# Kernel optimization log

Hardware: AMD Instinct MI355X
Metric: run time of the kernel (lower is better)

Reference implementation:

```python
import jax, jax.numpy as jnp
import numpy as np
import math

B, C, H, W = 16, 128, 64, 64

def _conv3(x, w, b):
    # 3x3 conv, padding=1 (SAME), NCHW / OIHW
    y = jax.lax.conv_general_dilated(x, w, window_strides=(1, 1), padding='SAME',
                                     dimension_numbers=('NCHW', 'OIHW', 'NCHW'))
    return y + b[None, :, None, None]

def setup_inputs() -> dict:
    key = jax.random.key(0)
    ks = jax.random.split(key, 12)
    s = 0.02
    inp = {
        'F_in': jax.random.normal(ks[0], (B, C, H, W), dtype=jnp.float32),
        'Pspe': jax.random.normal(ks[1], (B, C, C), dtype=jnp.float32),
        'q_w': jax.random.normal(ks[2], (C, C, 3, 3), dtype=jnp.float32) * s,
        'q_b': jnp.zeros((C,), dtype=jnp.float32),
        'k_w': jax.random.normal(ks[3], (C, C, 3, 3), dtype=jnp.float32) * s,
        'k_b': jnp.zeros((C,), dtype=jnp.float32),
        'v_w': jax.random.normal(ks[4], (C, C, 3, 3), dtype=jnp.float32) * s,
        'v_b': jnp.zeros((C,), dtype=jnp.float32),
        'f1_w': jax.random.normal(ks[5], (C, C, 3, 3), dtype=jnp.float32) * s,
        'f1_b': jnp.zeros((C,), dtype=jnp.float32),
        'f2_w': jax.random.normal(ks[6], (C, C, 3, 3), dtype=jnp.float32) * s,
        'f2_b': jnp.zeros((C,), dtype=jnp.float32),
    }
    return inp

def reference(F_in, Pspe, q_w, q_b, k_w, k_b, v_w, v_b, f1_w, f1_b, f2_w, f2_b):
    b, c, h, w = F_in.shape
    hw = h * w
    Qm = _conv3(F_in, q_w, q_b)
    Km = _conv3(F_in, k_w, k_b)
    Vm = _conv3(F_in, v_w, v_b)
    # (B,C,H,W) -> (B,HW,C)
    Q = jnp.transpose(Qm, (0, 2, 3, 1)).reshape(b, hw, c)
    K = jnp.transpose(Km, (0, 2, 3, 1)).reshape(b, hw, c)
    V = jnp.transpose(Vm, (0, 2, 3, 1)).reshape(b, hw, c)
    # channel-wise attention: (B,C,C) = K^T Q, contracting over HW
    attn_logits = jnp.einsum('bnc,bnd->bcd', K, Q) / math.sqrt(hw)
    A = jax.nn.softmax(attn_logits, axis=-1)
    M = jnp.einsum('bce,bed->bcd', Pspe, A)         # prompt fusion
    F3 = jnp.einsum('bnc,bcd->bnd', V, M)           # (B,HW,C)
    F3_map = jnp.transpose(F3.reshape(b, h, w, c), (0, 3, 1, 2))
    # MScanBlock is not defined in the provided source -> identity
    F_ssm = F3_map
    ffn = _conv3(jax.nn.gelu(_conv3(F_ssm, f1_w, f1_b), approximate=False), f2_w, f2_b)
    return F_ssm + ffn
```

## Files before the change

kernel.cpp:

```cpp
#include <hip/hip_runtime.h>
#include <cmath>

typedef unsigned short u16;
typedef __bf16 bf16x8 __attribute__((ext_vector_type(8)));
typedef float f32x4 __attribute__((ext_vector_type(4)));

__device__ __forceinline__ u16 f2bf(float f) {
  unsigned u = __float_as_uint(f);
  u += 0x7fffu + ((u >> 16) & 1u);
  return (u16)(u >> 16);
}
__device__ __forceinline__ float bf2f(u16 h) {
  return __uint_as_float(((unsigned)h) << 16);
}
__device__ __forceinline__ f32x4 mfma_bf16(bf16x8 a, bf16x8 b, f32x4 c) {
  return __builtin_amdgcn_mfma_f32_16x16x32_bf16(a, b, c, 0, 0, 0);
}
__device__ __forceinline__ float gelu_exact(float x) {
  return 0.5f * x * (1.0f + erff(x * 0.70710678118654752440f));
}


__global__ __launch_bounds__(256) void pack_x(const float* __restrict__ Fin,
                                              u16* __restrict__ X) {
  const int b = blockIdx.x >> 6, y = blockIdx.x & 63;
  const int tid = threadIdx.x;
  __shared__ float T[64 * 129];
#pragma unroll
  for (int i = 0; i < 32; ++i) {
    int idx = tid + i * 256;
    int c = idx >> 6, x = idx & 63;
    T[x * 129 + c] = Fin[(size_t)(b * 128 + c) * 4096 + y * 64 + x];
  }
  __syncthreads();
#pragma unroll
  for (int i = 0; i < 4; ++i) {
    int chunk = tid + i * 256;
    int x = chunk >> 4;
    int c0 = (chunk & 15) * 8;
    u16 tmp[8];
#pragma unroll
    for (int e = 0; e < 8; ++e) tmp[e] = f2bf(T[x * 129 + c0 + e]);
    *reinterpret_cast<uint4*>(X + ((size_t)((b * 64 + y) * 64 + x) * 128 + c0)) =
        *reinterpret_cast<const uint4*>(tmp);
  }
}

__global__ __launch_bounds__(256) void pack_w(const float* __restrict__ w0,
                                              const float* __restrict__ w1,
                                              const float* __restrict__ w2,
                                              const float* __restrict__ w3,
                                              const float* __restrict__ w4,
                                              u16* __restrict__ Wpk) {
  int gid = blockIdx.x * 256 + threadIdx.x;
  int lane = gid & 63;
  int nblk = (gid >> 6) & 7;
  int step = (gid >> 9) % 36;
  int conv = gid / (512 * 36);
  if (conv >= 5) return;
  const float* w = conv == 0 ? w0 : conv == 1 ? w1 : conv == 2 ? w2 : conv == 3 ? w3 : w4;
  int tap = step >> 2, cc = step & 3;
  int dy = tap / 3, dx = tap % 3;
  int co = nblk * 16 + (lane & 15);
  int ci0 = cc * 32 + (lane >> 4) * 8;
  u16 tmp[8];
#pragma unroll
  for (int e = 0; e < 8; ++e)
    tmp[e] = f2bf(w[((size_t)(co * 128 + ci0 + e) * 3 + dy) * 3 + dx]);
  size_t off = ((size_t)conv * 36 * 8 * 64 + (size_t)((step * 8 + nblk) * 64 + lane)) * 8;
  *reinterpret_cast<uint4*>(Wpk + off) = *reinterpret_cast<const uint4*>(tmp);
}

__device__ __forceinline__ void stage_tile(const u16* __restrict__ Xin, u16* Xs,
                                           int tid, int b, int y0) {
#pragma unroll
  for (int i = 0; i < 16; ++i) {
    int j = tid + i * 256;
    int row = j >> 4;
    int c16 = j & 15;
    int ys = row >> 6, x = row & 63;
    int ysrc = y0 - 1 + ys;
    uint4 val = make_uint4(0u, 0u, 0u, 0u);
    if ((unsigned)ysrc < 64u)
      val = *reinterpret_cast<const uint4*>(
          Xin + ((size_t)((b * 64 + ysrc) * 64 + x) * 128 + c16 * 8));
    int xs = x + 1;
    unsigned off = (unsigned)(((ys * 66 + xs) * 128 + c16 * 8) * 2) ^
                   (unsigned)((xs & 7) << 4);
    *reinterpret_cast<uint4*>(reinterpret_cast<char*>(Xs) + off) = val;
  }
  if (tid < 128) {
    int ys = tid >> 5, side = (tid >> 4) & 1, c16 = tid & 15;
    int xs = side ? 65 : 0;
    unsigned off = (unsigned)(((ys * 66 + xs) * 128 + c16 * 8) * 2) ^
                   (unsigned)((xs & 7) << 4);
    *reinterpret_cast<uint4*>(reinterpret_cast<char*>(Xs) + off) =
        make_uint4(0u, 0u, 0u, 0u);
  }
}

__device__ __forceinline__ void epi_pack(f32x4 (&acc)[4][4], const float* __restrict__ bias,
                                         u16* __restrict__ OutB, u16* T, int tid,
                                         int wm, int wn, int lm, int lq, int b, int mt) {
#pragma unroll
  for (int i = 0; i < 4; ++i)
#pragma unroll
    for (int j = 0; j < 4; ++j) {
      int n = wn * 64 + j * 16 + lm;
      float bs = bias[n];
#pragma unroll
      for (int r = 0; r < 4; ++r) {
        int m = wm * 64 + i * 16 + lq * 4 + r;
        T[n * 136 + m] = f2bf(acc[i][j][r] + bs);
      }
    }
  __syncthreads();
  const int ksbase = (mt & 31) * 4;
#pragma unroll
  for (int it = 0; it < 8; ++it) {
    int item = tid + it * 256;
    int l = item & 63, cb = (item >> 6) & 7, ksl = item >> 9;
    int c = cb * 16 + (l & 15);
    int mloc = ksl * 32 + (l >> 4) * 8;
    *reinterpret_cast<uint4*>(
        OutB + (size_t)(((b * 128 + ksbase + ksl) * 8 + cb) * 64 + l) * 8) =
        *reinterpret_cast<const uint4*>(T + c * 136 + mloc);
  }
  __syncthreads();
}

__device__ __forceinline__ void epi_nat(f32x4 (&acc)[4][4], const float* __restrict__ bias,
                                        u16* __restrict__ OutB, u16* T, int tid,
                                        int wm, int wn, int lm, int lq, int mt) {
#pragma unroll
  for (int i = 0; i < 4; ++i)
#pragma unroll
    for (int j = 0; j < 4; ++j) {
      int n = wn * 64 + j * 16 + lm;
      float bs = bias[n];
#pragma unroll
      for (int r = 0; r < 4; ++r) {
        int m = wm * 64 + i * 16 + lq * 4 + r;
        T[m * 136 + n] = f2bf(acc[i][j][r] + bs);
      }
    }
  __syncthreads();
  int rr = tid >> 1, hf = tid & 1;
  const uint4* src = reinterpret_cast<const uint4*>(T + rr * 136 + hf * 64);
  uint4* dst = reinterpret_cast<uint4*>(OutB + ((size_t)(mt * 128 + rr) * 128 + hf * 64));
#pragma unroll
  for (int k = 0; k < 8; ++k) dst[k] = src[k];
  __syncthreads();
}

__global__ __launch_bounds__(256, 2) void conv_qkv(
    const u16* __restrict__ Xin, const u16* __restrict__ Wp,
    const float* __restrict__ qb, const float* __restrict__ kb,
    const float* __restrict__ vb, u16* __restrict__ QP,
    u16* __restrict__ KP, u16* __restrict__ Vout) {
  __shared__ alignas(16) u16 Xs[4 * 66 * 128];
  const int tid = threadIdx.x;
  const int lane = tid & 63;
  const int wv = tid >> 6;
  const int wm = wv >> 1, wn = wv & 1;
  int mt = blockIdx.x;
  mt = (mt & 7) * 64 + (mt >> 3);
  const int b = mt >> 5;
  const int y0 = (mt & 31) * 2;

  stage_tile(Xin, Xs, tid, b, y0);
  __syncthreads();

  f32x4 acc[3][4][4];
#pragma unroll
  for (int c = 0; c < 3; ++c)
#pragma unroll
    for (int i = 0; i < 4; ++i)
#pragma unroll
      for (int j = 0; j < 4; ++j) acc[c][i][j] = f32x4{0.f, 0.f, 0.f, 0.f};

  const int lm = lane & 15, lq = lane >> 4;

#pragma unroll 1
  for (int tap = 0; tap < 9; ++tap) {
    const int dy = (tap * 11) >> 5;
    const int dx = tap - dy * 3;
    const int ysrow = (wm + dy) * 66;
#pragma unroll
    for (int cc = 0; cc < 4; ++cc) {
      const int step = tap * 4 + cc;
      bf16x8 af[4];
#pragma unroll
      for (int i = 0; i < 4; ++i) {
        int xs = i * 16 + lm + dx;
        unsigned off = (unsigned)(((ysrow + xs) * 128 + cc * 32 + lq * 8) * 2) ^
                       (unsigned)((xs & 7) << 4);
        af[i] = *reinterpret_cast<const bf16x8*>(
            reinterpret_cast<const char*>(Xs) + off);
      }
#pragma unroll
      for (int cv = 0; cv < 3; ++cv) {
        const u16* wl = Wp + (size_t)cv * 147456 + (size_t)lane * 8;
        bf16x8 bfr[4];
#pragma unroll
        for (int j = 0; j < 4; ++j)
          bfr[j] = *reinterpret_cast<const bf16x8*>(
              wl + (size_t)((step * 8 + wn * 4 + j) * 64) * 8);
#pragma unroll
        for (int i = 0; i < 4; ++i)
#pragma unroll
          for (int j = 0; j < 4; ++j)
            acc[cv][i][j] = mfma_bf16(af[i], bfr[j], acc[cv][i][j]);
      }
    }
  }

  __syncthreads();
  epi_pack(acc[0], qb, QP, Xs, tid, wm, wn, lm, lq, b, mt);
  epi_pack(acc[1], kb, KP, Xs, tid, wm, wn, lm, lq, b, mt);
  epi_nat(acc[2], vb, Vout, Xs, tid, wm, wn, lm, lq, mt);
}

template <int MODE>
__global__ __launch_bounds__(256, 2) void conv_gemm(
    const u16* __restrict__ Xin, const u16* __restrict__ Wp,
    const float* __restrict__ bias, u16* __restrict__ OutB,
    float* __restrict__ OutF, const u16* __restrict__ Fssm) {
  __shared__ alignas(16) u16 Xs[4 * 66 * 128];
  const int tid = threadIdx.x;
  const int lane = tid & 63;
  const int wv = tid >> 6;
  const int wm = wv >> 1, wn = wv & 1;
  int mt = blockIdx.x;
  mt = (mt & 7) * 64 + (mt >> 3);
  const int b = mt >> 5;
  const int y0 = (mt & 31) * 2;

  stage_tile(Xin, Xs, tid, b, y0);
  __syncthreads();

  f32x4 acc[4][4];
#pragma unroll
  for (int i = 0; i < 4; ++i)
#pragma unroll
    for (int j = 0; j < 4; ++j) acc[i][j] = f32x4{0.f, 0.f, 0.f, 0.f};

  const int lm = lane & 15, lq = lane >> 4;
  const u16* wlane = Wp + (size_t)lane * 8;

#pragma unroll
  for (int tap = 0; tap < 9; ++tap) {
    const int dy = tap / 3, dx = tap % 3;
    const int ysrow = (wm + dy) * 66;
#pragma unroll
    for (int cc = 0; cc < 4; ++cc) {
      const int step = tap * 4 + cc;
      bf16x8 af[4], bfr[4];
#pragma unroll
      for (int i = 0; i < 4; ++i) {
        int xs = i * 16 + lm + dx;
        unsigned off = (unsigned)(((ysrow + xs) * 128 + cc * 32 + lq * 8) * 2) ^
                       (unsigned)((xs & 7) << 4);
        af[i] = *reinterpret_cast<const bf16x8*>(
            reinterpret_cast<const char*>(Xs) + off);
      }
#pragma unroll
      for (int j = 0; j < 4; ++j)
        bfr[j] = *reinterpret_cast<const bf16x8*>(
            wlane + (size_t)((step * 8 + wn * 4 + j) * 64) * 8);
#pragma unroll
      for (int i = 0; i < 4; ++i)
#pragma unroll
        for (int j = 0; j < 4; ++j) acc[i][j] = mfma_bf16(af[i], bfr[j], acc[i][j]);
    }
  }

  __syncthreads();

  if (MODE == 1) {
    u16* T = Xs;
#pragma unroll
    for (int i = 0; i < 4; ++i)
#pragma unroll
      for (int j = 0; j < 4; ++j) {
        int n = wn * 64 + j * 16 + lm;
        float bs = bias[n];
#pragma unroll
        for (int r = 0; r < 4; ++r) {
          int m = wm * 64 + i * 16 + lq * 4 + r;
          T[m * 136 + n] = f2bf(gelu_exact(acc[i][j][r] + bs));
        }
      }
    __syncthreads();
    int rr = tid >> 1, hf = tid & 1;
    const uint4* src = reinterpret_cast<const uint4*>(T + rr * 136 + hf * 64);
    uint4* dst = reinterpret_cast<uint4*>(OutB + ((size_t)(mt * 128 + rr) * 128 + hf * 64));
#pragma unroll
    for (int k = 0; k < 8; ++k) dst[k] = src[k];
  } else {
    float* T = reinterpret_cast<float*>(Xs);
#pragma unroll
    for (int i = 0; i < 4; ++i)
#pragma unroll
      for (int j = 0; j < 4; ++j) {
        int n = wn * 64 + j * 16 + lm;
        float bs = bias[n];
#pragma unroll
        for (int r = 0; r < 4; ++r) {
          int m = wm * 64 + i * 16 + lq * 4 + r;
          float v = acc[i][j][r] + bs + bf2f(Fssm[(size_t)(mt * 128 + m) * 128 + n]);
          T[n * 132 + m] = v;
        }
      }
    __syncthreads();
    int rr = tid >> 1, hf = tid & 1;
    const uint4* src = reinterpret_cast<const uint4*>(T + rr * 132 + hf * 64);
    uint4* dst = reinterpret_cast<uint4*>(
        OutF + ((size_t)(b * 128 + rr) * 4096 + (mt & 31) * 128 + hf * 64));
#pragma unroll
    for (int k = 0; k < 16; ++k) dst[k] = src[k];
  }
}

__global__ __launch_bounds__(256, 2) void attn_s(const u16* __restrict__ QP,
                                                 const u16* __restrict__ KP,
                                                 float* __restrict__ SP) {
  const int tid = threadIdx.x;
  const int lane = tid & 63;
  const int wv = tid >> 6, wm = wv >> 1, wn = wv & 1;
  const int lm = lane & 15, lq = lane >> 4;
  int mt = blockIdx.x;
  mt = (mt & 7) * 16 + (mt >> 3);
  const int b = mt >> 3, sp = mt & 7;

  f32x4 acc[4][4];
#pragma unroll
  for (int i = 0; i < 4; ++i)
#pragma unroll
    for (int j = 0; j < 4; ++j) acc[i][j] = f32x4{0.f, 0.f, 0.f, 0.f};

#pragma unroll
  for (int ksl = 0; ksl < 16; ++ksl) {
    const int ks = sp * 16 + ksl;
    bf16x8 af[4], bfr[4];
#pragma unroll
    for (int i = 0; i < 4; ++i)
      af[i] = *reinterpret_cast<const bf16x8*>(
          KP + (size_t)(((b * 128 + ks) * 8 + wm * 4 + i) * 64 + lane) * 8);
#pragma unroll
    for (int j = 0; j < 4; ++j)
      bfr[j] = *reinterpret_cast<const bf16x8*>(
          QP + (size_t)(((b * 128 + ks) * 8 + wn * 4 + j) * 64 + lane) * 8);
#pragma unroll
    for (int i = 0; i < 4; ++i)
#pragma unroll
      for (int j = 0; j < 4; ++j) acc[i][j] = mfma_bf16(af[i], bfr[j], acc[i][j]);
  }

  float* out = SP + (size_t)(b * 8 + sp) * 16384;
#pragma unroll
  for (int i = 0; i < 4; ++i)
#pragma unroll
    for (int j = 0; j < 4; ++j)
#pragma unroll
      for (int r = 0; r < 4; ++r)
        out[(wm * 64 + i * 16 + lq * 4 + r) * 128 + wn * 64 + j * 16 + lm] =
            acc[i][j][r];
}

__global__ __launch_bounds__(256) void attn_r(const float* __restrict__ SP,
                                              u16* __restrict__ ABP) {
  __shared__ float Sf[32][129];
  __shared__ float Inv[32];
  const int tid = threadIdx.x;
  const int b = blockIdx.x >> 2, eb = blockIdx.x & 3;

#pragma unroll
  for (int it = 0; it < 16; ++it) {
    int id = it * 256 + tid;
    int rl = id >> 7, d = id & 127;
    const float* p = SP + (size_t)b * 8 * 16384 + (size_t)(eb * 32 + rl) * 128 + d;
    float s = 0.f;
#pragma unroll
    for (int sp = 0; sp < 8; ++sp) s += p[(size_t)sp * 16384];
    Sf[rl][d] = s * 0.015625f;
  }
  __syncthreads();

  {
    int rl = tid >> 3, sub = tid & 7;
    float mx = -3.4e38f;
#pragma unroll
    for (int k = 0; k < 16; ++k) mx = fmaxf(mx, Sf[rl][sub + 8 * k]);
    mx = fmaxf(mx, __shfl_xor(mx, 1));
    mx = fmaxf(mx, __shfl_xor(mx, 2));
    mx = fmaxf(mx, __shfl_xor(mx, 4));
    float s = 0.f;
#pragma unroll
    for (int k = 0; k < 16; ++k) {
      float e = __expf(Sf[rl][sub + 8 * k] - mx);
      Sf[rl][sub + 8 * k] = e;
      s += e;
    }
    s += __shfl_xor(s, 1);
    s += __shfl_xor(s, 2);
    s += __shfl_xor(s, 4);
    if (sub == 0) Inv[rl] = 1.0f / s;
  }
  __syncthreads();

#pragma unroll
  for (int it = 0; it < 2; ++it) {
    int item = tid + it * 256;
    int l = item & 63, nb = item >> 6;
    int d = nb * 16 + (l & 15);
    u16 tmp[8];
#pragma unroll
    for (int e = 0; e < 8; ++e) {
      int rloc = (l >> 4) * 8 + e;
      tmp[e] = f2bf(Sf[rloc][d] * Inv[rloc]);
    }
    *reinterpret_cast<uint4*>(ABP + (size_t)(((b * 4 + eb) * 8 + nb) * 64 + l) * 8) =
        *reinterpret_cast<const uint4*>(tmp);
  }
}

__global__ __launch_bounds__(256, 1) void attn_m(const float* __restrict__ Pspe,
                                                 const u16* __restrict__ ABP,
                                                 u16* __restrict__ Mpack) {
  __shared__ u16 Ml[128 * 136];
  const int b = blockIdx.x;
  const int tid = threadIdx.x;
  const int lane = tid & 63;
  const int wv = tid >> 6, wm = wv >> 1, wn = wv & 1;
  const int lm = lane & 15, lq = lane >> 4;

  f32x4 acc[4][4];
#pragma unroll
  for (int i = 0; i < 4; ++i)
#pragma unroll
    for (int j = 0; j < 4; ++j) acc[i][j] = f32x4{0.f, 0.f, 0.f, 0.f};

  const float* P = Pspe + (size_t)b * 128 * 128;
#pragma unroll
  for (int cc = 0; cc < 4; ++cc) {
    int e0 = cc * 32 + lq * 8;
    bf16x8 af[4], bfr[4];
#pragma unroll
    for (int i = 0; i < 4; ++i) {
      const float* p = P + (size_t)(wm * 64 + i * 16 + lm) * 128 + e0;
      union { u16 u[8]; bf16x8 v; } cv;
#pragma unroll
      for (int e = 0; e < 8; ++e) cv.u[e] = f2bf(p[e]);
      af[i] = cv.v;
    }
#pragma unroll
    for (int j = 0; j < 4; ++j)
      bfr[j] = *reinterpret_cast<const bf16x8*>(
          ABP + (size_t)(((b * 4 + cc) * 8 + wn * 4 + j) * 64 + lane) * 8);
#pragma unroll
    for (int i = 0; i < 4; ++i)
#pragma unroll
      for (int j = 0; j < 4; ++j) acc[i][j] = mfma_bf16(af[i], bfr[j], acc[i][j]);
  }

#pragma unroll
  for (int i = 0; i < 4; ++i)
#pragma unroll
    for (int j = 0; j < 4; ++j)
#pragma unroll
      for (int r = 0; r < 4; ++r)
        Ml[(wn * 64 + j * 16 + lm) * 136 + (wm * 64 + i * 16 + lq * 4 + r)] =
            f2bf(acc[i][j][r]);
  __syncthreads();

#pragma unroll
  for (int it = 0; it < 8; ++it) {
    int item = tid + it * 256;
    int l2 = item & 63, nb = (item >> 6) & 7, cc2 = item >> 9;
    int d = nb * 16 + (l2 & 15), c0 = cc2 * 32 + (l2 >> 4) * 8;
    *reinterpret_cast<uint4*>(Mpack + (size_t)b * 16384 + (size_t)item * 8) =
        *reinterpret_cast<const uint4*>(Ml + d * 136 + c0);
  }
}

__global__ __launch_bounds__(256) void f3_gemm(const u16* __restrict__ V,
                                               const u16* __restrict__ Mpack,
                                               u16* __restrict__ Fout) {
  const int tid = threadIdx.x;
  const int lane = tid & 63;
  const int wv = tid >> 6, wm = wv >> 1, wn = wv & 1;
  const int lm = lane & 15, lq = lane >> 4;
  int mt = blockIdx.x;
  mt = (mt & 7) * 64 + (mt >> 3);
  const int b = mt >> 5;

  f32x4 acc[4][4];
#pragma unroll
  for (int i = 0; i < 4; ++i)
#pragma unroll
    for (int j = 0; j < 4; ++j) acc[i][j] = f32x4{0.f, 0.f, 0.f, 0.f};

#pragma unroll
  for (int cc = 0; cc < 4; ++cc) {
    int k0 = cc * 32 + lq * 8;
    bf16x8 af[4], bfr[4];
#pragma unroll
    for (int i = 0; i < 4; ++i)
      af[i] = *reinterpret_cast<const bf16x8*>(
          V + (size_t)(mt * 128 + wm * 64 + i * 16 + lm) * 128 + k0);
#pragma unroll
    for (int j = 0; j < 4; ++j)
      bfr[j] = *reinterpret_cast<const bf16x8*>(
          Mpack + (size_t)b * 16384 + (size_t)((cc * 8 + wn * 4 + j) * 64 + lane) * 8);
#pragma unroll
    for (int i = 0; i < 4; ++i)
#pragma unroll
      for (int j = 0; j < 4; ++j) acc[i][j] = mfma_bf16(af[i], bfr[j], acc[i][j]);
  }

  __shared__ u16 T[128 * 136];
#pragma unroll
  for (int i = 0; i < 4; ++i)
#pragma unroll
    for (int j = 0; j < 4; ++j)
#pragma unroll
      for (int r = 0; r < 4; ++r)
        T[(wm * 64 + i * 16 + lq * 4 + r) * 136 + wn * 64 + j * 16 + lm] =
            f2bf(acc[i][j][r]);
  __syncthreads();
  int rr = tid >> 1, hf = tid & 1;
  const uint4* src = reinterpret_cast<const uint4*>(T + rr * 136 + hf * 64);
  uint4* dst = reinterpret_cast<uint4*>(Fout + ((size_t)(mt * 128 + rr) * 128 + hf * 64));
#pragma unroll
  for (int k = 0; k < 8; ++k) dst[k] = src[k];
}

extern "C" void kernel_launch(void* const* d_in, const int* in_sizes, int n_in,
                              void* d_out, int out_size, void* d_ws, size_t ws_size,
                              hipStream_t stream) {
  const float* F_in = (const float*)d_in[0];
  const float* Pspe = (const float*)d_in[1];
  const float* q_w = (const float*)d_in[2];
  const float* q_b = (const float*)d_in[3];
  const float* k_w = (const float*)d_in[4];
  const float* k_b = (const float*)d_in[5];
  const float* v_w = (const float*)d_in[6];
  const float* v_b = (const float*)d_in[7];
  const float* f1_w = (const float*)d_in[8];
  const float* f1_b = (const float*)d_in[9];
  const float* f2_w = (const float*)d_in[10];
  const float* f2_b = (const float*)d_in[11];
  float* out = (float*)d_out;

  char* ws = (char*)d_ws;
  const size_t SZ = 16777216;
  u16* X = (u16*)(ws);
  u16* QP = (u16*)(ws + SZ);
  u16* KP = (u16*)(ws + 2 * SZ);
  u16* V = (u16*)(ws + 3 * SZ);
  u16* Wpk = (u16*)(ws + 4 * SZ);
  u16* Mpk = (u16*)(ws + 4 * SZ + 1474560);
  float* SP = (float*)ws;
  u16* ABP = KP;
  u16* Fssm = X;
  u16* Hid = QP;

  pack_x<<<1024, 256, 0, stream>>>(F_in, X);
  pack_w<<<360, 256, 0, stream>>>(q_w, k_w, v_w, f1_w, f2_w, Wpk);
  conv_qkv<<<512, 256, 0, stream>>>(X, Wpk, q_b, k_b, v_b, QP, KP, V);
  attn_s<<<128, 256, 0, stream>>>(QP, KP, SP);
  attn_r<<<64, 256, 0, stream>>>(SP, ABP);
  attn_m<<<16, 256, 0, stream>>>(Pspe, ABP, Mpk);
  f3_gemm<<<512, 256, 0, stream>>>(V, Mpk, Fssm);
  conv_gemm<1><<<512, 256, 0, stream>>>(Fssm, Wpk + 3 * 147456, f1_b, Hid, nullptr, nullptr);
  conv_gemm<3><<<512, 256, 0, stream>>>(Hid, Wpk + 4 * 147456, f2_b, nullptr, out, Fssm);
}
```

Baseline: 182.4 us.

## Merge pack kernels, split QKV conv over output halves, double-buffer fragment loads

Merges the input and weight packing kernels into one launch to save a launch gap. Splits conv_qkv so each block computes only half of the output channels, doubling the grid to 1024 blocks and halving the accumulator registers per thread. Adds a two-stage software pipeline for LDS and weight fragment loads in both conv kernels so loads overlap with MFMA work. The cost is that each input tile is staged twice (once per channel half) and the epilogues become more complex.

Result: faster. 176.9 us (-3.0%).

```diff
diff --git a/kernel.cpp b/kernel.cpp
--- a/kernel.cpp
+++ b/kernel.cpp
@@ -21,54 +21,52 @@
 }
 
 
-__global__ __launch_bounds__(256) void pack_x(const float* __restrict__ Fin,
-                                              u16* __restrict__ X) {
-  const int b = blockIdx.x >> 6, y = blockIdx.x & 63;
+__global__ __launch_bounds__(256) void pack_xw(
+    const float* __restrict__ Fin, u16* __restrict__ X,
+    const float* __restrict__ w0, const float* __restrict__ w1,
+    const float* __restrict__ w2, const float* __restrict__ w3,
+    const float* __restrict__ w4, u16* __restrict__ Wpk) {
+  __shared__ float T[64 * 129];
   const int tid = threadIdx.x;
-  __shared__ float T[64 * 129];
-#pragma unroll
-  for (int i = 0; i < 32; ++i) {
-    int idx = tid + i * 256;
-    int c = idx >> 6, x = idx & 63;
-    T[x * 129 + c] = Fin[(size_t)(b * 128 + c) * 4096 + y * 64 + x];
-  }
-  __syncthreads();
-#pragma unroll
-  for (int i = 0; i < 4; ++i) {
-    int chunk = tid + i * 256;
-    int x = chunk >> 4;
-    int c0 = (chunk & 15) * 8;
+  if (blockIdx.x < 1024) {
+    const int b = blockIdx.x >> 6, y = blockIdx.x & 63;
+#pragma unroll
+    for (int i = 0; i < 32; ++i) {
+      int idx = tid + i * 256;
+      int c = idx >> 6, x = idx & 63;
+      T[x * 129 + c] = Fin[(size_t)(b * 128 + c) * 4096 + y * 64 + x];
+    }
+    __syncthreads();
+#pragma unroll
+    for (int i = 0; i < 4; ++i) {
+      int chunk = tid + i * 256;
+      int x = chunk >> 4;
+      int c0 = (chunk & 15) * 8;
+      u16 tmp[8];
+#pragma unroll
+      for (int e = 0; e < 8; ++e) tmp[e] = f2bf(T[x * 129 + c0 + e]);
+      *reinterpret_cast<uint4*>(X + ((size_t)((b * 64 + y) * 64 + x) * 128 + c0)) =
+          *reinterpret_cast<const uint4*>(tmp);
+    }
+  } else {
+    int gid = (blockIdx.x - 1024) * 256 + tid;
+    int lane = gid & 63;
+    int nblk = (gid >> 6) & 7;
+    int step = (gid >> 9) % 36;
+    int conv = gid / (512 * 36);
+    if (conv >= 5) return;
+    const float* w = conv == 0 ? w0 : conv == 1 ? w1 : conv == 2 ? w2 : conv == 3 ? w3 : w4;
+    int tap = step >> 2, cc = step & 3;
+    int dy = tap / 3, dx = tap % 3;
+    int co = nblk * 16 + (lane & 15);
+    int ci0 = cc * 32 + (lane >> 4) * 8;
     u16 tmp[8];
 #pragma unroll
-    for (int e = 0; e < 8; ++e) tmp[e] = f2bf(T[x * 129 + c0 + e]);
-    *reinterpret_cast<uint4*>(X + ((size_t)((b * 64 + y) * 64 + x) * 128 + c0)) =
-        *reinterpret_cast<const uint4*>(tmp);
-  }
-}
-
-__global__ __launch_bounds__(256) void pack_w(const float* __restrict__ w0,
-                                              const float* __restrict__ w1,
-                                              const float* __restrict__ w2,
-                                              const float* __restrict__ w3,
-                                              const float* __restrict__ w4,
-                                              u16* __restrict__ Wpk) {
-  int gid = blockIdx.x * 256 + threadIdx.x;
-  int lane = gid & 63;
-  int nblk = (gid >> 6) & 7;
-  int step = (gid >> 9) % 36;
-  int conv = gid / (512 * 36);
-  if (conv >= 5) return;
-  const float* w = conv == 0 ? w0 : conv == 1 ? w1 : conv == 2 ? w2 : conv == 3 ? w3 : w4;
-  int tap = step >> 2, cc = step & 3;
-  int dy = tap / 3, dx = tap % 3;
-  int co = nblk * 16 + (lane & 15);
-  int ci0 = cc * 32 + (lane >> 4) * 8;
-  u16 tmp[8];
-#pragma unroll
-  for (int e = 0; e < 8; ++e)
-    tmp[e] = f2bf(w[((size_t)(co * 128 + ci0 + e) * 3 + dy) * 3 + dx]);
-  size_t off = ((size_t)conv * 36 * 8 * 64 + (size_t)((step * 8 + nblk) * 64 + lane)) * 8;
-  *reinterpret_cast<uint4*>(Wpk + off) = *reinterpret_cast<const uint4*>(tmp);
+    for (int e = 0; e < 8; ++e)
+      tmp[e] = f2bf(w[((size_t)(co * 128 + ci0 + e) * 3 + dy) * 3 + dx]);
+    size_t off = ((size_t)conv * 36 * 8 * 64 + (size_t)((step * 8 + nblk) * 64 + lane)) * 8;
+    *reinterpret_cast<uint4*>(Wpk + off) = *reinterpret_cast<const uint4*>(tmp);
+  }
 }
 
 __device__ __forceinline__ void stage_tile(const u16* __restrict__ Xin, u16* Xs,
@@ -99,60 +97,6 @@
   }
 }
 
-__device__ __forceinline__ void epi_pack(f32x4 (&acc)[4][4], const float* __restrict__ bias,
-                                         u16* __restrict__ OutB, u16* T, int tid,
-                                         int wm, int wn, int lm, int lq, int b, int mt) {
-#pragma unroll
-  for (int i = 0; i < 4; ++i)
-#pragma unroll
-    for (int j = 0; j < 4; ++j) {
-      int n = wn * 64 + j * 16 + lm;
-      float bs = bias[n];
-#pragma unroll
-      for (int r = 0; r < 4; ++r) {
-        int m = wm * 64 + i * 16 + lq * 4 + r;
-        T[n * 136 + m] = f2bf(acc[i][j][r] + bs);
-      }
-    }
-  __syncthreads();
-  const int ksbase = (mt & 31) * 4;
-#pragma unroll
-  for (int it = 0; it < 8; ++it) {
-    int item = tid + it * 256;
-    int l = item & 63, cb = (item >> 6) & 7, ksl = item >> 9;
-    int c = cb * 16 + (l & 15);
-    int mloc = ksl * 32 + (l >> 4) * 8;
-    *reinterpret_cast<uint4*>(
-        OutB + (size_t)(((b * 128 + ksbase + ksl) * 8 + cb) * 64 + l) * 8) =
-        *reinterpret_cast<const uint4*>(T + c * 136 + mloc);
-  }
-  __syncthreads();
-}
-
-__device__ __forceinline__ void epi_nat(f32x4 (&acc)[4][4], const float* __restrict__ bias,
-                                        u16* __restrict__ OutB, u16* T, int tid,
-                                        int wm, int wn, int lm, int lq, int mt) {
-#pragma unroll
-  for (int i = 0; i < 4; ++i)
-#pragma unroll
-    for (int j = 0; j < 4; ++j) {
-      int n = wn * 64 + j * 16 + lm;
-      float bs = bias[n];
-#pragma unroll
-      for (int r = 0; r < 4; ++r) {
-        int m = wm * 64 + i * 16 + lq * 4 + r;
-        T[m * 136 + n] = f2bf(acc[i][j][r] + bs);
-      }
-    }
-  __syncthreads();
-  int rr = tid >> 1, hf = tid & 1;
-  const uint4* src = reinterpret_cast<const uint4*>(T + rr * 136 + hf * 64);
-  uint4* dst = reinterpret_cast<uint4*>(OutB + ((size_t)(mt * 128 + rr) * 128 + hf * 64));
-#pragma unroll
-  for (int k = 0; k < 8; ++k) dst[k] = src[k];
-  __syncthreads();
-}
-
 __global__ __launch_bounds__(256, 2) void conv_qkv(
     const u16* __restrict__ Xin, const u16* __restrict__ Wp,
     const float* __restrict__ qb, const float* __restrict__ kb,
@@ -164,61 +108,129 @@
   const int wv = tid >> 6;
   const int wm = wv >> 1, wn = wv & 1;
   int mt = blockIdx.x;
-  mt = (mt & 7) * 64 + (mt >> 3);
-  const int b = mt >> 5;
-  const int y0 = (mt & 31) * 2;
+  mt = (mt & 7) * 128 + (mt >> 3);
+  const int b = mt >> 6;
+  const int r = mt & 63;
+  const int yp = r >> 1;
+  const int nh = r & 1;
+  const int y0 = yp * 2;
 
   stage_tile(Xin, Xs, tid, b, y0);
   __syncthreads();
 
-  f32x4 acc[3][4][4];
+  f32x4 acc[3][4][2];
 #pragma unroll
   for (int c = 0; c < 3; ++c)
 #pragma unroll
     for (int i = 0; i < 4; ++i)
 #pragma unroll
-      for (int j = 0; j < 4; ++j) acc[c][i][j] = f32x4{0.f, 0.f, 0.f, 0.f};
+      for (int j = 0; j < 2; ++j) acc[c][i][j] = f32x4{0.f, 0.f, 0.f, 0.f};
 
   const int lm = lane & 15, lq = lane >> 4;
-
+  const u16* wb = Wp + (size_t)(((nh * 4 + wn * 2) * 64) + lane) * 8;
+
+  auto loada = [&](bf16x8 (&d)[4], int s) {
+    int tap = s >> 2, cc = s & 3;
+    int dy = (tap * 11) >> 5;
+    int dx = tap - dy * 3;
+    int row = (wm + dy) * 66;
+#pragma unroll
+    for (int i = 0; i < 4; ++i) {
+      int xs = i * 16 + lm + dx;
+      unsigned off = (unsigned)(((row + xs) * 128 + cc * 32 + lq * 8) * 2) ^
+                     (unsigned)((xs & 7) << 4);
+      d[i] = *reinterpret_cast<const bf16x8*>(reinterpret_cast<const char*>(Xs) + off);
+    }
+  };
+  auto loadb = [&](bf16x8 (&d)[6], int s) {
+#pragma unroll
+    for (int cv = 0; cv < 3; ++cv)
+#pragma unroll
+      for (int j = 0; j < 2; ++j)
+        d[cv * 2 + j] = *reinterpret_cast<const bf16x8*>(
+            wb + (size_t)cv * 147456 + (size_t)s * 4096 + j * 512);
+  };
+  auto step = [&](bf16x8 (&a)[4], bf16x8 (&bm)[6]) {
+#pragma unroll
+    for (int cv = 0; cv < 3; ++cv)
+#pragma unroll
+      for (int i = 0; i < 4; ++i)
+#pragma unroll
+        for (int j = 0; j < 2; ++j)
+          acc[cv][i][j] = mfma_bf16(a[i], bm[cv * 2 + j], acc[cv][i][j]);
+  };
+
+  bf16x8 a0[4], a1[4], b0[6], b1[6];
+  loada(a0, 0);
+  loadb(b0, 0);
 #pragma unroll 1
-  for (int tap = 0; tap < 9; ++tap) {
-    const int dy = (tap * 11) >> 5;
-    const int dx = tap - dy * 3;
-    const int ysrow = (wm + dy) * 66;
-#pragma unroll
-    for (int cc = 0; cc < 4; ++cc) {
-      const int step = tap * 4 + cc;
-      bf16x8 af[4];
-#pragma unroll
-      for (int i = 0; i < 4; ++i) {
-        int xs = i * 16 + lm + dx;
-        unsigned off = (unsigned)(((ysrow + xs) * 128 + cc * 32 + lq * 8) * 2) ^
-                       (unsigned)((xs & 7) << 4);
-        af[i] = *reinterpret_cast<const bf16x8*>(
-            reinterpret_cast<const char*>(Xs) + off);
+  for (int s = 0; s < 36; s += 2) {
+    loada(a1, s + 1);
+    loadb(b1, s + 1);
+    step(a0, b0);
+    if (s + 2 < 36) {
+      loada(a0, s + 2);
+      loadb(b0, s + 2);
+    }
+    step(a1, b1);
+  }
+
+  __syncthreads();
+
+  u16* T = Xs;
+#pragma unroll
+  for (int cv = 0; cv < 2; ++cv) {
+    const float* bias = cv == 0 ? qb : kb;
+    u16* OutB = cv == 0 ? QP : KP;
+#pragma unroll
+    for (int i = 0; i < 4; ++i)
+#pragma unroll
+      for (int j = 0; j < 2; ++j) {
+        int nloc = wn * 32 + j * 16 + lm;
+        float bs = bias[nh * 64 + nloc];
+#pragma unroll
+        for (int rr = 0; rr < 4; ++rr) {
+          int m = wm * 64 + i * 16 + lq * 4 + rr;
+          T[nloc * 136 + m] = f2bf(acc[cv][i][j][rr] + bs);
+        }
       }
-#pragma unroll
-      for (int cv = 0; cv < 3; ++cv) {
-        const u16* wl = Wp + (size_t)cv * 147456 + (size_t)lane * 8;
-        bf16x8 bfr[4];
-#pragma unroll
-        for (int j = 0; j < 4; ++j)
-          bfr[j] = *reinterpret_cast<const bf16x8*>(
-              wl + (size_t)((step * 8 + wn * 4 + j) * 64) * 8);
-#pragma unroll
-        for (int i = 0; i < 4; ++i)
-#pragma unroll
-          for (int j = 0; j < 4; ++j)
-            acc[cv][i][j] = mfma_bf16(af[i], bfr[j], acc[cv][i][j]);
+    __syncthreads();
+#pragma unroll
+    for (int it = 0; it < 4; ++it) {
+      int item = tid + it * 256;
+      int l = item & 63, cbl = (item >> 6) & 3, ksl = item >> 8;
+      int c = cbl * 16 + (l & 15);
+      int mloc = ksl * 32 + (l >> 4) * 8;
+      int ks = yp * 4 + ksl, cb = nh * 4 + cbl;
+      *reinterpret_cast<uint4*>(
+          OutB + (size_t)(((b * 128 + ks) * 8 + cb) * 64 + l) * 8) =
+          *reinterpret_cast<const uint4*>(T + c * 136 + mloc);
+    }
+    __syncthreads();
+  }
+
+  u16* Tv = Xs;
+#pragma unroll
+  for (int i = 0; i < 4; ++i)
+#pragma unroll
+    for (int j = 0; j < 2; ++j) {
+      int nloc = wn * 32 + j * 16 + lm;
+      float bs = vb[nh * 64 + nloc];
+#pragma unroll
+      for (int rr = 0; rr < 4; ++rr) {
+        int m = wm * 64 + i * 16 + lq * 4 + rr;
+        Tv[m * 72 + nloc] = f2bf(acc[2][i][j][rr] + bs);
       }
     }
-  }
-
-  __syncthreads();
-  epi_pack(acc[0], qb, QP, Xs, tid, wm, wn, lm, lq, b, mt);
-  epi_pack(acc[1], kb, KP, Xs, tid, wm, wn, lm, lq, b, mt);
-  epi_nat(acc[2], vb, Vout, Xs, tid, wm, wn, lm, lq, mt);
+  __syncthreads();
+  {
+    int rr = tid >> 1, q = tid & 1;
+    const uint4* src = reinterpret_cast<const uint4*>(Tv + rr * 72 + q * 32);
+    uint4* dst = reinterpret_cast<uint4*>(
+        Vout + ((size_t)((b * 32 + yp) * 128 + rr) * 128 + nh * 64 + q * 32));
+#pragma unroll
+    for (int k = 0; k < 4; ++k) dst[k] = src[k];
+  }
 }
 
 template <int MODE>
@@ -246,33 +258,46 @@
     for (int j = 0; j < 4; ++j) acc[i][j] = f32x4{0.f, 0.f, 0.f, 0.f};
 
   const int lm = lane & 15, lq = lane >> 4;
-  const u16* wlane = Wp + (size_t)lane * 8;
-
-#pragma unroll
-  for (int tap = 0; tap < 9; ++tap) {
-    const int dy = tap / 3, dx = tap % 3;
-    const int ysrow = (wm + dy) * 66;
-#pragma unroll
-    for (int cc = 0; cc < 4; ++cc) {
-      const int step = tap * 4 + cc;
-      bf16x8 af[4], bfr[4];
-#pragma unroll
-      for (int i = 0; i < 4; ++i) {
-        int xs = i * 16 + lm + dx;
-        unsigned off = (unsigned)(((ysrow + xs) * 128 + cc * 32 + lq * 8) * 2) ^
-                       (unsigned)((xs & 7) << 4);
-        af[i] = *reinterpret_cast<const bf16x8*>(
-            reinterpret_cast<const char*>(Xs) + off);
-      }
-#pragma unroll
-      for (int j = 0; j < 4; ++j)
-        bfr[j] = *reinterpret_cast<const bf16x8*>(
-            wlane + (size_t)((step * 8 + wn * 4 + j) * 64) * 8);
-#pragma unroll
-      for (int i = 0; i < 4; ++i)
-#pragma unroll
-        for (int j = 0; j < 4; ++j) acc[i][j] = mfma_bf16(af[i], bfr[j], acc[i][j]);
-    }
+  const u16* wb = Wp + (size_t)((wn * 4 * 64) + lane) * 8;
+
+  auto loada = [&](bf16x8 (&d)[4], int s) {
+    int tap = s >> 2, cc = s & 3;
+    int dy = (tap * 11) >> 5;
+    int dx = tap - dy * 3;
+    int row = (wm + dy) * 66;
+#pragma unroll
+    for (int i = 0; i < 4; ++i) {
+      int xs = i * 16 + lm + dx;
+      unsigned off = (unsigned)(((row + xs) * 128 + cc * 32 + lq * 8) * 2) ^
+                     (unsigned)((xs & 7) << 4);
+      d[i] = *reinterpret_cast<const bf16x8*>(reinterpret_cast<const char*>(Xs) + off);
+    }
+  };
+  auto loadb = [&](bf16x8 (&d)[4], int s) {
+#pragma unroll
+    for (int j = 0; j < 4; ++j)
+      d[j] = *reinterpret_cast<const bf16x8*>(wb + (size_t)s * 4096 + j * 512);
+  };
+  auto step = [&](bf16x8 (&a)[4], bf16x8 (&bm)[4]) {
+#pragma unroll
+    for (int i = 0; i < 4; ++i)
+#pragma unroll
+      for (int j = 0; j < 4; ++j) acc[i][j] = mfma_bf16(a[i], bm[j], acc[i][j]);
+  };
+
+  bf16x8 a0[4], a1[4], b0[4], b1[4];
+  loada(a0, 0);
+  loadb(b0, 0);
+#pragma unroll 1
+  for (int s = 0; s < 36; s += 2) {
+    loada(a1, s + 1);
+    loadb(b1, s + 1);
+    step(a0, b0);
+    if (s + 2 < 36) {
+      loada(a0, s + 2);
+      loadb(b0, s + 2);
+    }
+    step(a1, b1);
   }
 
   __syncthreads();
@@ -566,9 +591,8 @@
   u16* Fssm = X;
   u16* Hid = QP;
 
-  pack_x<<<1024, 256, 0, stream>>>(F_in, X);
-  pack_w<<<360, 256, 0, stream>>>(q_w, k_w, v_w, f1_w, f2_w, Wpk);
-  conv_qkv<<<512, 256, 0, stream>>>(X, Wpk, q_b, k_b, v_b, QP, KP, V);
+  pack_xw<<<1384, 256, 0, stream>>>(F_in, X, q_w, k_w, v_w, f1_w, f2_w, Wpk);
+  conv_qkv<<<1024, 256, 0, stream>>>(X, Wpk, q_b, k_b, v_b, QP, KP, V);
   attn_s<<<128, 256, 0, stream>>>(QP, KP, SP);
   attn_r<<<64, 256, 0, stream>>>(SP, ABP);
   attn_m<<<16, 256, 0, stream>>>(Pspe, ABP, Mpk);
```
